# Performance work log

Hardware: AMD Instinct MI355X
Metric: run time of the kernel (lower is better)

## Reference

```python
import jax, jax.numpy as jnp
import numpy as np

D, NQ, BS, NL, NH, NP, DFF = 256, 900, 8, 4, 8, 4, 1024
HD = D // NH
SHAPES = np.array([[100, 100], [50, 50], [25, 25], [13, 13]], dtype=np.int64)  # (H, W) per level
LSTART = np.concatenate([[0], np.cumsum(SHAPES[:, 0] * SHAPES[:, 1])[:-1]]).astype(np.int64)
LMEM = int((SHAPES[:, 0] * SHAPES[:, 1]).sum())


def layer_norm(x, g, b, eps=1e-5):
    mu = x.mean(-1, keepdims=True)
    var = ((x - mu) ** 2).mean(-1, keepdims=True)
    return (x - mu) * jax.lax.rsqrt(var + eps) * g + b


def _forward(tgt, tgt_query_pos, tgt_reference_points, memory,
             in_proj_w, in_proj_b, out_proj_w, out_proj_b,
             samp_off_w, samp_off_b, attn_w_w, attn_w_b,
             value_proj_w, value_proj_b, output_proj_w, output_proj_b,
             lin1_w, lin1_b, lin2_w, lin2_b,
             norm1_g, norm1_b, norm2_g, norm2_b, norm3_g, norm3_b):
    # ---- self-attention (seq-first, torch nn.MultiheadAttention semantics) ----
    q = tgt + tgt_query_pos  # q = k = with_pos_embed(tgt, pos)
    Wq, Wk, Wv = jnp.split(in_proj_w, 3, 0)
    bq, bk, bv = jnp.split(in_proj_b, 3, 0)
    def heads(x):  # (nq, bs, d) -> (bs, nh, nq, hd)
        return x.reshape(NQ, BS, NH, HD).transpose(1, 2, 0, 3)
    qh = heads(q @ Wq.T + bq)
    kh = heads(q @ Wk.T + bk)
    vh = heads(tgt @ Wv.T + bv)
    attn = jax.nn.softmax(jnp.einsum('bhqd,bhkd->bhqk', qh, kh) / np.float32(np.sqrt(HD)), -1)
    sa = jnp.einsum('bhqk,bhkd->bhqd', attn, vh).transpose(2, 0, 1, 3).reshape(NQ, BS, D)
    sa = sa @ out_proj_w.T + out_proj_b
    t = layer_norm(tgt + sa, norm2_g, norm2_b)

    # ---- MSDeformAttn cross-attention (batch-first internally) ----
    qb = (t + tgt_query_pos).transpose(1, 0, 2)          # (bs, nq, d)
    refb = tgt_reference_points.transpose(1, 0, 2, 3)    # (bs, nq, nl, 2) in [0,1]
    memb = memory.transpose(1, 0, 2)                     # (bs, L, d)
    value = (memb @ value_proj_w.T + value_proj_b).reshape(BS, LMEM, NH, HD)
    off = (qb @ samp_off_w.T + samp_off_b).reshape(BS, NQ, NH, NL, NP, 2)
    aw = jax.nn.softmax((qb @ attn_w_w.T + attn_w_b).reshape(BS, NQ, NH, NL * NP), -1)
    aw = aw.reshape(BS, NQ, NH, NL, NP)
    normz = jnp.asarray(SHAPES[:, ::-1].copy(), dtype=jnp.float32)  # (nl, 2) = [W, H]
    loc = refb[:, :, None, :, None, :] + off / normz[None, None, None, :, None, :]

    out = jnp.zeros((BS, NQ, NH, HD), jnp.float32)
    for l in range(NL):  # fixed small number of pyramid levels
        Hl, Wl = int(SHAPES[l, 0]), int(SHAPES[l, 1])
        s = int(LSTART[l])
        v_l = value[:, s:s + Hl * Wl]  # (bs, Hl*Wl, nh, hd)
        # grid_sample(align_corners=False, padding=zeros) pixel coords
        x = (loc[:, :, :, l, :, 0] * Wl - 0.5).transpose(0, 1, 3, 2).reshape(BS, NQ * NP, NH)
        y = (loc[:, :, :, l, :, 1] * Hl - 0.5).transpose(0, 1, 3, 2).reshape(BS, NQ * NP, NH)
        x0 = jnp.floor(x)
        y0 = jnp.floor(y)
        samp = jnp.zeros((BS, NQ * NP, NH, HD), jnp.float32)
        for dx in (0, 1):
            for dy in (0, 1):
                xc = x0 + dx
                yc = y0 + dy
                w = (1.0 - jnp.abs(x - xc)) * (1.0 - jnp.abs(y - yc))
                valid = (xc >= 0) & (xc < Wl) & (yc >= 0) & (yc < Hl)
                idx = (jnp.clip(yc, 0, Hl - 1) * Wl + jnp.clip(xc, 0, Wl - 1)).astype(jnp.int32)
                g = jnp.take_along_axis(v_l, idx[..., None], axis=1)  # (bs, nq*np, nh, hd)
                samp = samp + jnp.where(valid, w, 0.0)[..., None] * g
        samp = samp.reshape(BS, NQ, NP, NH, HD)
        out = out + jnp.einsum('bqhp,bqphd->bqhd', aw[:, :, :, l], samp)
    ca = (out.reshape(BS, NQ, D) @ output_proj_w.T + output_proj_b).transpose(1, 0, 2)
    t = layer_norm(t + ca, norm1_g, norm1_b)

    # ---- FFN ----
    ffn = jax.nn.relu(t @ lin1_w.T + lin1_b) @ lin2_w.T + lin2_b
    return layer_norm(t + ffn, norm3_g, norm3_b)


def setup_inputs() -> dict:
    key = jax.random.key(0)
    ks = jax.random.split(key, 24)
    r = lambda i, shape, s: jax.random.normal(ks[i], shape, jnp.float32) * s
    return {
        'tgt': r(0, (NQ, BS, D), 1.0),
        'tgt_query_pos': r(1, (NQ, BS, D), 1.0),
        'tgt_reference_points': jax.random.uniform(ks[2], (NQ, BS, NL, 2), jnp.float32),
        'memory': r(3, (LMEM, BS, D), 1.0),
        'spatial_shapes': jnp.asarray(SHAPES),
        'level_start_index': jnp.asarray(LSTART),
        'in_proj_w': r(4, (3 * D, D), 0.02), 'in_proj_b': r(5, (3 * D,), 0.02),
        'out_proj_w': r(6, (D, D), 0.02), 'out_proj_b': r(7, (D,), 0.02),
        'samp_off_w': r(8, (NH * NL * NP * 2, D), 0.01), 'samp_off_b': r(9, (NH * NL * NP * 2,), 0.01),
        'attn_w_w': r(10, (NH * NL * NP, D), 0.02), 'attn_w_b': r(11, (NH * NL * NP,), 0.02),
        'value_proj_w': r(12, (D, D), 0.02), 'value_proj_b': r(13, (D,), 0.02),
        'output_proj_w': r(14, (D, D), 0.02), 'output_proj_b': r(15, (D,), 0.02),
        'lin1_w': r(16, (DFF, D), 0.02), 'lin1_b': r(17, (DFF,), 0.02),
        'lin2_w': r(18, (D, DFF), 0.02), 'lin2_b': r(19, (D,), 0.02),
        'norm1_g': jnp.ones((D,), jnp.float32), 'norm1_b': jnp.zeros((D,), jnp.float32),
        'norm2_g': jnp.ones((D,), jnp.float32), 'norm2_b': jnp.zeros((D,), jnp.float32),
        'norm3_g': jnp.ones((D,), jnp.float32), 'norm3_b': jnp.zeros((D,), jnp.float32),
    }


def reference(tgt, tgt_query_pos, tgt_reference_points, memory, spatial_shapes, level_start_index,
              in_proj_w, in_proj_b, out_proj_w, out_proj_b, samp_off_w, samp_off_b,
              attn_w_w, attn_w_b, value_proj_w, value_proj_b, output_proj_w, output_proj_b,
              lin1_w, lin1_b, lin2_w, lin2_b, norm1_g, norm1_b, norm2_g, norm2_b, norm3_g, norm3_b):
    # spatial_shapes / level_start_index are static level constants (module-level SHAPES/LSTART)
    return _forward(tgt, tgt_query_pos, tgt_reference_points, memory,
                    in_proj_w, in_proj_b, out_proj_w, out_proj_b,
                    samp_off_w, samp_off_b, attn_w_w, attn_w_b,
                    value_proj_w, value_proj_b, output_proj_w, output_proj_b,
                    lin1_w, lin1_b, lin2_w, lin2_b,
                    norm1_g, norm1_b, norm2_g, norm2_b, norm3_g, norm3_b)
```

## Files before the change

kernel.cpp:

```cpp
#include <hip/hip_runtime.h>
#include <hip/hip_bf16.h>


namespace {
constexpr int D_ = 256;
constexpr int NQ_ = 900;
constexpr int BS_ = 8;
constexpr int NH_ = 8;
constexpr int HD_ = 32;
constexpr int DFF_ = 1024;
constexpr int MTOK = NQ_ * BS_;
constexpr int LMEM_ = 13294;
constexpr long T = (long)MTOK * D_;
constexpr float QSC = 0.17677669529663687f;
constexpr int QKS = 512;
}

typedef __attribute__((ext_vector_type(8))) short bf8_t;
typedef __attribute__((ext_vector_type(4))) float f4_t;

#define MFMA16(a, b, c) __builtin_amdgcn_mfma_f32_16x16x32_bf16((a), (b), (c), 0, 0, 0)

__device__ __forceinline__ unsigned short bfbits(float x) {
    union { __hip_bfloat16 h; unsigned short u; } cv;
    cv.h = __float2bfloat16(x);
    return cv.u;
}
__device__ __forceinline__ float bf2f(unsigned short u) {
    union { float f; unsigned v; } cv;
    cv.v = ((unsigned)u) << 16;
    return cv.f;
}

__device__ __forceinline__ void gload16(const unsigned short* g, unsigned short* l) {
    __builtin_amdgcn_global_load_lds(
        (const __attribute__((address_space(1))) unsigned int*)(g),
        (__attribute__((address_space(3))) unsigned int*)(l), 16, 0, 0);
}

__global__ void prep_inputs(const float* __restrict__ tgt, const float* __restrict__ pos,
                            unsigned short* __restrict__ tgt_bf,
                            unsigned short* __restrict__ qplus_bf, long n4) {
    const long i = (long)blockIdx.x * blockDim.x + threadIdx.x;
    if (i < n4) {
        const float4 tv = ((const float4*)tgt)[i];
        const float4 pv = ((const float4*)pos)[i];
        union { unsigned short u[4]; uint2 w; } a, b;
        a.u[0] = bfbits(tv.x); a.u[1] = bfbits(tv.y); a.u[2] = bfbits(tv.z); a.u[3] = bfbits(tv.w);
        b.u[0] = bfbits(tv.x + pv.x); b.u[1] = bfbits(tv.y + pv.y);
        b.u[2] = bfbits(tv.z + pv.z); b.u[3] = bfbits(tv.w + pv.w);
        ((uint2*)tgt_bf)[i] = a.w;
        ((uint2*)qplus_bf)[i] = b.w;
    }
}

__global__ void permute_mem(const float* __restrict__ mem, unsigned short* __restrict__ dst) {
    const long idx = (long)blockIdx.x * 256 + threadIdx.x;
    const int d4 = (int)(idx & 63);
    const int b = (int)((idx >> 6) & 7);
    const long i = idx >> 9;
    const float4 v = ((const float4*)mem)[idx];
    union { unsigned short u[4]; uint2 w; } pk;
    pk.u[0] = bfbits(v.x); pk.u[1] = bfbits(v.y); pk.u[2] = bfbits(v.z); pk.u[3] = bfbits(v.w);
    *(uint2*)(dst + (((long)b * LMEM_ + i) * D_ + d4 * 4)) = pk.w;
}

__global__ void conv_weights(
    const float* __restrict__ ipw, const float* __restrict__ opw,
    const float* __restrict__ sow, const float* __restrict__ aww,
    const float* __restrict__ vpw, const float* __restrict__ outpw,
    const float* __restrict__ l1w, const float* __restrict__ l2w,
    const float* __restrict__ ipb, const float* __restrict__ sob,
    const float* __restrict__ awb,
    unsigned short* __restrict__ Wbf, float* __restrict__ biasAll)
{
    if (blockIdx.x == 0) {
        for (int j = threadIdx.x; j < 512; j += 256)
            biasAll[j] = (j < 256) ? ipb[j] * QSC : ipb[j];
        for (int j = threadIdx.x; j < 384; j += 256)
            biasAll[512 + j] = (j < 256) ? sob[j] : awb[j - 256];
    }
    const long idx4 = (long)blockIdx.x * 256 + threadIdx.x;
    if (idx4 >= 253952) return;
    const long e = idx4 * 4;
    const float* src; long off; float sc = 1.f;
    if (e < 196608)      { src = ipw;   off = 0;      if (e < 65536) sc = QSC; }
    else if (e < 262144) { src = opw;   off = 196608; }
    else if (e < 327680) { src = sow;   off = 262144; }
    else if (e < 360448) { src = aww;   off = 327680; }
    else if (e < 425984) { src = vpw;   off = 360448; }
    else if (e < 491520) { src = outpw; off = 425984; }
    else if (e < 753664) { src = l1w;   off = 491520; }
    else                 { src = l2w;   off = 753664; }
    const float4 v = *(const float4*)(src + (e - off));
    union { unsigned short u[4]; uint2 w; } pk;
    pk.u[0] = bfbits(v.x * sc); pk.u[1] = bfbits(v.y * sc);
    pk.u[2] = bfbits(v.z * sc); pk.u[3] = bfbits(v.w * sc);
    *(uint2*)(Wbf + e) = pk.w;
}

template<bool RELU, bool OUTBF16>
__global__ __launch_bounds__(256) void gemm_mfma(
    const unsigned short* __restrict__ A, const unsigned short* __restrict__ W,
    const float* __restrict__ bias, void* __restrict__ C, int M, int N, int K)
{
    __shared__ unsigned short As[128 * 32];
    __shared__ unsigned short Ws[128 * 32];
    const int t = threadIdx.x;
    const long m0 = (long)blockIdx.x * 128;
    const int n0 = blockIdx.y * 128;
    const int row0 = t >> 2, cg = t & 3;
    long ar0 = m0 + row0;        if (ar0 > M - 1) ar0 = M - 1;
    long ar1 = m0 + 64 + row0;   if (ar1 > M - 1) ar1 = M - 1;
    const unsigned short* ga0 = A + ar0 * K + cg * 8;
    const unsigned short* ga1 = A + ar1 * K + cg * 8;
    const unsigned short* gw0 = W + (long)(n0 + row0) * K + cg * 8;
    const unsigned short* gw1 = W + (long)(n0 + 64 + row0) * K + cg * 8;
    unsigned short* la0 = As + t * 8;
    unsigned short* la1 = As + 2048 + t * 8;
    unsigned short* lw0 = Ws + t * 8;
    unsigned short* lw1 = Ws + 2048 + t * 8;
    const int lane = t & 63, wave = t >> 6;
    const int c = lane & 15, g = lane >> 4;
    const int wr = wave >> 1, wc = wave & 1;
    f4_t acc[4][4];
#pragma unroll
    for (int i = 0; i < 4; ++i)
#pragma unroll
        for (int j = 0; j < 4; ++j)
            acc[i][j] = f4_t{0.f, 0.f, 0.f, 0.f};

    for (int kb = 0; kb < K; kb += 32) {
        gload16(ga0 + kb, la0);
        gload16(ga1 + kb, la1);
        gload16(gw0 + kb, lw0);
        gload16(gw1 + kb, lw1);
        __syncthreads();
        bf8_t af[4], bfr[4];
#pragma unroll
        for (int i = 0; i < 4; ++i) {
            af[i] = *(const bf8_t*)(As + (wr * 64 + i * 16 + c) * 32 + g * 8);
            bfr[i] = *(const bf8_t*)(Ws + (wc * 64 + i * 16 + c) * 32 + g * 8);
        }
#pragma unroll
        for (int i = 0; i < 4; ++i)
#pragma unroll
            for (int j = 0; j < 4; ++j)
                acc[i][j] = MFMA16(af[i], bfr[j], acc[i][j]);
        __syncthreads();
    }

#pragma unroll
    for (int i = 0; i < 4; ++i) {
        const long rbase = m0 + wr * 64 + i * 16 + 4 * g;
#pragma unroll
        for (int j = 0; j < 4; ++j) {
            const int col = n0 + wc * 64 + j * 16 + c;
            const float bv = bias[col];
#pragma unroll
            for (int r = 0; r < 4; ++r) {
                const long rr = rbase + r;
                if (rr < M) {
                    float v = acc[i][j][r] + bv;
                    if (RELU) v = fmaxf(v, 0.f);
                    if (OUTBF16) ((unsigned short*)C)[rr * N + col] = bfbits(v);
                    else         ((float*)C)[rr * N + col] = v;
                }
            }
        }
    }
}

__global__ __launch_bounds__(256) void attn_mfma(
    const unsigned short* __restrict__ Qb, const unsigned short* __restrict__ Kb,
    const unsigned short* __restrict__ Vb, unsigned short* __restrict__ sa)
{
    __shared__ float smemf[2112];
    unsigned short* Ks = (unsigned short*)smemf;
    unsigned short* Vt = (unsigned short*)(smemf + 1024);
    const int t = threadIdx.x;
    const int wave = t >> 6, lane = t & 63;
    const int g = lane >> 4, c = lane & 15;
    const int b = blockIdx.x >> 3, h = blockIdx.x & 7;
    const int q0 = blockIdx.y * 64 + wave * 16;
    const int q = q0 + c;
    const bool qv = q < NQ_;
    const bf8_t qf = *(const bf8_t*)(Qb + ((long)(qv ? q : 0) * BS_ + b) * QKS + h * HD_ + 8 * g);

    f4_t acc0 = {0.f, 0.f, 0.f, 0.f}, acc1 = {0.f, 0.f, 0.f, 0.f};
    float m_run = -1e30f, l_run = 0.f;
    const int sk = t >> 2, sd = (t & 3) * 8;

    for (int kc = 0; kc < NQ_; kc += 64) {
        __syncthreads();
        {
            const int key = kc + sk;
            union { bf8_t v; unsigned short u[8]; } kv, vv;
            if (key < NQ_) {
                kv.v = *(const bf8_t*)(Kb + ((long)key * BS_ + b) * QKS + h * HD_ + sd);
                vv.v = *(const bf8_t*)(Vb + ((long)key * BS_ + b) * D_ + h * HD_ + sd);
            } else {
#pragma unroll
                for (int u = 0; u < 8; ++u) { kv.u[u] = 0; vv.u[u] = 0; }
            }
            *(bf8_t*)(Ks + sk * 32 + sd) = kv.v;
#pragma unroll
            for (int u = 0; u < 8; ++u) {
                const int r = sd + u;
                Vt[r * 64 + (sk ^ ((r & 7) << 3))] = vv.u[u];
            }
        }
        __syncthreads();

        f4_t s[4];
#pragma unroll
        for (int tt = 0; tt < 4; ++tt) {
            const bf8_t kf = *(const bf8_t*)(Ks + (tt * 16 + c) * 32 + 8 * g);
            f4_t z = {0.f, 0.f, 0.f, 0.f};
            s[tt] = MFMA16(kf, qf, z);
        }
        float sv[16];
#pragma unroll
        for (int tt = 0; tt < 4; ++tt)
#pragma unroll
            for (int r = 0; r < 4; ++r) {
                float x = s[tt][r];
                if (kc + tt * 16 + 4 * g + r >= NQ_) x = -1e30f;
                sv[tt * 4 + r] = x;
            }
        float mloc = sv[0];
#pragma unroll
        for (int i = 1; i < 16; ++i) mloc = fmaxf(mloc, sv[i]);
        mloc = fmaxf(mloc, __shfl_xor(mloc, 16));
        mloc = fmaxf(mloc, __shfl_xor(mloc, 32));
        const float mnew = fmaxf(m_run, mloc);
        const float resc = __expf(m_run - mnew);
        float p[16], ls = 0.f;
#pragma unroll
        for (int i = 0; i < 16; ++i) { p[i] = __expf(sv[i] - mnew); ls += p[i]; }
        ls += __shfl_xor(ls, 16);
        ls += __shfl_xor(ls, 32);
        l_run = l_run * resc + ls;
        m_run = mnew;
#pragma unroll
        for (int r = 0; r < 4; ++r) { acc0[r] *= resc; acc1[r] *= resc; }

        unsigned pk[4][2];
#pragma unroll
        for (int tt = 0; tt < 4; ++tt) {
            pk[tt][0] = (unsigned)bfbits(p[tt * 4 + 0]) | ((unsigned)bfbits(p[tt * 4 + 1]) << 16);
            pk[tt][1] = (unsigned)bfbits(p[tt * 4 + 2]) | ((unsigned)bfbits(p[tt * 4 + 3]) << 16);
        }
        const int srcA = ((g & 1) << 5) + c;
        const int srcB = srcA + 16;
#pragma unroll
        for (int kh = 0; kh < 2; ++kh) {
            const unsigned a0 = __shfl(pk[kh * 2][0], srcA), b0_ = __shfl(pk[kh * 2 + 1][0], srcA);
            const unsigned a1 = __shfl(pk[kh * 2][1], srcA), b1_ = __shfl(pk[kh * 2 + 1][1], srcA);
            const unsigned a2 = __shfl(pk[kh * 2][0], srcB), b2_ = __shfl(pk[kh * 2 + 1][0], srcB);
            const unsigned a3 = __shfl(pk[kh * 2][1], srcB), b3_ = __shfl(pk[kh * 2 + 1][1], srcB);
            union { bf8_t v; unsigned u[4]; } pf;
            const bool hi = (g & 2);
            pf.u[0] = hi ? b0_ : a0; pf.u[1] = hi ? b1_ : a1;
            pf.u[2] = hi ? b2_ : a2; pf.u[3] = hi ? b3_ : a3;
            const int kcol = (kh * 32 + 8 * g) ^ ((c & 7) << 3);
            const bf8_t vf0 = *(const bf8_t*)(Vt + c * 64 + kcol);
            const bf8_t vf1 = *(const bf8_t*)(Vt + (16 + c) * 64 + kcol);
            acc0 = MFMA16(vf0, pf.v, acc0);
            acc1 = MFMA16(vf1, pf.v, acc1);
        }
    }

    __syncthreads();
    const float invl = 1.f / l_run;
    float* O = smemf + wave * 528;
#pragma unroll
    for (int r = 0; r < 4; ++r) {
        O[c * 33 + 4 * g + r] = acc0[r] * invl;
        O[c * 33 + 16 + 4 * g + r] = acc1[r] * invl;
    }
    __syncthreads();
    {
        const int ql = lane >> 2, part = lane & 3;
        const int qg = q0 + ql;
        if (qg < NQ_) {
            union { bf8_t v; unsigned short u[8]; } pk;
#pragma unroll
            for (int u = 0; u < 8; ++u) pk.u[u] = bfbits(O[ql * 33 + part * 8 + u]);
            *(bf8_t*)(sa + ((long)qg * BS_ + b) * D_ + h * HD_ + part * 8) = pk.v;
        }
    }
}

__global__ __launch_bounds__(256) void msdeform_kernel(
    const float* __restrict__ oa, const float* __restrict__ refp,
    const unsigned short* __restrict__ val, unsigned short* __restrict__ out)
{
    __shared__ float saw[128];
    __shared__ float redm[8], redi[8];
    __shared__ float swt[128][4];
    __shared__ int sidx[128][4];
    const int bq = blockIdx.x;
    const int b = bq / NQ_, q = bq % NQ_;
    const int t = threadIdx.x;
    if (t < 128) saw[t] = oa[(long)bq * 384 + 256 + t];
    __syncthreads();
    if (t < 8) {
        float mx = -1e30f;
        for (int i = 0; i < 16; ++i) mx = fmaxf(mx, saw[t * 16 + i]);
        float s = 0.f;
        for (int i = 0; i < 16; ++i) s += __expf(saw[t * 16 + i] - mx);
        redm[t] = mx; redi[t] = 1.f / s;
    }
    __syncthreads();
    if (t < 128) {
        const int h = t >> 4, lp = t & 15, l = lp >> 2, p = lp & 3;
        const float aw = __expf(saw[t] - redm[h]) * redi[h];
        const int Wi = (l == 0) ? 100 : (l == 1) ? 50 : (l == 2) ? 25 : 13;
        const int Hi = Wi;
        const int sl = (l == 0) ? 0 : (l == 1) ? 10000 : (l == 2) ? 12500 : 13125;
        const float offx = oa[(long)bq * 384 + h * 32 + l * 8 + p * 2 + 0];
        const float offy = oa[(long)bq * 384 + h * 32 + l * 8 + p * 2 + 1];
        const float refx = refp[(((long)q * BS_ + b) * 4 + l) * 2 + 0];
        const float refy = refp[(((long)q * BS_ + b) * 4 + l) * 2 + 1];
        const float fW = (float)Wi, fH = (float)Hi;
        const float x = (refx + offx / fW) * fW - 0.5f;
        const float y = (refy + offy / fH) * fH - 0.5f;
        const float x0f = floorf(x), y0f = floorf(y);
        const float fx = x - x0f, fy = y - y0f;
        const int ix = (int)x0f, iy = (int)y0f;
        const float wts[4] = {(1.f - fx) * (1.f - fy), fx * (1.f - fy),
                              (1.f - fx) * fy,          fx * fy};
        const int xs[4] = {ix, ix + 1, ix, ix + 1};
        const int ys[4] = {iy, iy, iy + 1, iy + 1};
#pragma unroll
        for (int tap = 0; tap < 4; ++tap) {
            const bool valid = (xs[tap] >= 0) & (xs[tap] < Wi) & (ys[tap] >= 0) & (ys[tap] < Hi);
            const int xc = min(max(xs[tap], 0), Wi - 1);
            const int yc = min(max(ys[tap], 0), Hi - 1);
            swt[t][tap] = valid ? aw * wts[tap] : 0.f;
            sidx[t][tap] = b * LMEM_ + sl + yc * Wi + xc;
        }
    }
    __syncthreads();
    const int h = t >> 5, r = t & 31, qd = r & 7, s = r >> 3;
    float a0 = 0.f, a1 = 0.f, a2 = 0.f, a3 = 0.f;
#pragma unroll
    for (int i = 0; i < 16; ++i) {
        const int j = h * 16 + i;
        const float wv = swt[j][s];
        const long base = (long)sidx[j][s] * D_ + h * HD_ + qd * 4;
        const uint2 raw = *(const uint2*)(val + base);
        a0 += wv * bf2f((unsigned short)(raw.x & 0xffff));
        a1 += wv * bf2f((unsigned short)(raw.x >> 16));
        a2 += wv * bf2f((unsigned short)(raw.y & 0xffff));
        a3 += wv * bf2f((unsigned short)(raw.y >> 16));
    }
    a0 += __shfl_xor(a0, 8); a0 += __shfl_xor(a0, 16);
    a1 += __shfl_xor(a1, 8); a1 += __shfl_xor(a1, 16);
    a2 += __shfl_xor(a2, 8); a2 += __shfl_xor(a2, 16);
    a3 += __shfl_xor(a3, 8); a3 += __shfl_xor(a3, 16);
    if (s == 0) {
        union { unsigned short u[4]; uint2 w; } pk;
        pk.u[0] = bfbits(a0); pk.u[1] = bfbits(a1); pk.u[2] = bfbits(a2); pk.u[3] = bfbits(a3);
        *(uint2*)(out + (long)bq * D_ + h * HD_ + qd * 4) = pk.w;
    }
}

__global__ __launch_bounds__(256) void ln_kernel(
    const float* __restrict__ inA, const float* __restrict__ inB,
    const float* __restrict__ g, const float* __restrict__ be,
    float* __restrict__ out, const float* __restrict__ pos,
    unsigned short* __restrict__ bfOut, int swapB, int bfMode)
{
    const int r = blockIdx.x * 4 + (threadIdx.x >> 6);
    const int lane = threadIdx.x & 63;
    long rb = r;
    if (swapB) rb = (long)(r & 7) * NQ_ + (r >> 3);
    const float4 a4 = *(const float4*)(inA + (long)r * D_ + lane * 4);
    const float4 b4 = *(const float4*)(inB + rb * D_ + lane * 4);
    float x[4] = {a4.x + b4.x, a4.y + b4.y, a4.z + b4.z, a4.w + b4.w};
    float s = x[0] + x[1] + x[2] + x[3];
#pragma unroll
    for (int off = 32; off > 0; off >>= 1) s += __shfl_xor(s, off);
    const float mu = s * (1.f / D_);
    float v = 0.f;
#pragma unroll
    for (int cc = 0; cc < 4; ++cc) { const float dd = x[cc] - mu; v += dd * dd; }
#pragma unroll
    for (int off = 32; off > 0; off >>= 1) v += __shfl_xor(v, off);
    const float rs = rsqrtf(v * (1.f / D_) + 1e-5f);
    const float4 g4 = *(const float4*)(g + lane * 4);
    const float4 e4 = *(const float4*)(be + lane * 4);
    const float gg[4] = {g4.x, g4.y, g4.z, g4.w};
    const float ee[4] = {e4.x, e4.y, e4.z, e4.w};
    float y[4];
#pragma unroll
    for (int cc = 0; cc < 4; ++cc) y[cc] = (x[cc] - mu) * rs * gg[cc] + ee[cc];
    *(float4*)(out + (long)r * D_ + lane * 4) = make_float4(y[0], y[1], y[2], y[3]);
    if (bfMode) {
        float z[4] = {y[0], y[1], y[2], y[3]};
        long er = r;
        if (bfMode == 2) {
            const float4 p4 = *(const float4*)(pos + (long)r * D_ + lane * 4);
            z[0] += p4.x; z[1] += p4.y; z[2] += p4.z; z[3] += p4.w;
            er = (long)(r & 7) * NQ_ + (r >> 3);
        }
        union { unsigned short u[4]; uint2 w; } pk;
        pk.u[0] = bfbits(z[0]); pk.u[1] = bfbits(z[1]);
        pk.u[2] = bfbits(z[2]); pk.u[3] = bfbits(z[3]);
        *(uint2*)(bfOut + er * D_ + lane * 4) = pk.w;
    }
}

extern "C" void kernel_launch(void* const* d_in, const int* in_sizes, int n_in,
                              void* d_out, int out_size, void* d_ws, size_t ws_size,
                              hipStream_t stream) {
    const float* tgt   = (const float*)d_in[0];
    const float* pos   = (const float*)d_in[1];
    const float* refp  = (const float*)d_in[2];
    const float* mem   = (const float*)d_in[3];
    const float* ipw   = (const float*)d_in[6];
    const float* ipb   = (const float*)d_in[7];
    const float* opw   = (const float*)d_in[8];
    const float* opb   = (const float*)d_in[9];
    const float* sow   = (const float*)d_in[10];
    const float* sob   = (const float*)d_in[11];
    const float* aww   = (const float*)d_in[12];
    const float* awb   = (const float*)d_in[13];
    const float* vpw   = (const float*)d_in[14];
    const float* vpb   = (const float*)d_in[15];
    const float* outpw = (const float*)d_in[16];
    const float* outpb = (const float*)d_in[17];
    const float* l1w   = (const float*)d_in[18];
    const float* l1b   = (const float*)d_in[19];
    const float* l2w   = (const float*)d_in[20];
    const float* l2b   = (const float*)d_in[21];
    const float* n1g = (const float*)d_in[22]; const float* n1be = (const float*)d_in[23];
    const float* n2g = (const float*)d_in[24]; const float* n2be = (const float*)d_in[25];
    const float* n3g = (const float*)d_in[26]; const float* n3be = (const float*)d_in[27];

    char* wsb = (char*)d_ws;
    auto alloc = [&](size_t bytes) { char* p = wsb; wsb += (bytes + 255) & ~(size_t)255; return p; };
    unsigned short* Wbf      = (unsigned short*)alloc(1015808 * 2);
    float*          biasAll  = (float*)alloc(896 * 4);
    unsigned short* tgt_bf   = (unsigned short*)alloc(T * 2);
    unsigned short* qplus_bf = (unsigned short*)alloc(T * 2);
    unsigned short* QK_bf    = (unsigned short*)alloc(T * 4);
    unsigned short* Vb_bf    = (unsigned short*)alloc(T * 2);
    unsigned short* sa_bf    = (unsigned short*)alloc(T * 2);
    float*          saproj   = (float*)alloc(T * 4);
    float*          t1       = (float*)alloc(T * 4);
    unsigned short* memT     = (unsigned short*)alloc((long)BS_ * LMEM_ * D_ * 2);
    unsigned short* val      = (unsigned short*)alloc((long)BS_ * LMEM_ * D_ * 2);
    unsigned short* qplus2_bf = qplus_bf;
    unsigned short* sampo_bf  = tgt_bf;
    float*          oa        = (float*)sa_bf;
    float*          t2        = (float*)(QK_bf + T);
    unsigned short* t2_bf     = QK_bf;
    unsigned short* ffnh_bf   = memT;
    float*          ffno      = (float*)((char*)memT + (long)MTOK * DFF_ * 2);
    float*          ca        = (float*)((char*)ffno + T * 4);
    const unsigned short* wqk = Wbf + 0;
    const unsigned short* wv  = Wbf + 131072;
    const unsigned short* wo  = Wbf + 196608;
    const unsigned short* wsoaw = Wbf + 262144;
    const unsigned short* wvp = Wbf + 360448;
    const unsigned short* wop = Wbf + 425984;
    const unsigned short* wl1 = Wbf + 491520;
    const unsigned short* wl2 = Wbf + 753664;
    const float* bias_qk = biasAll;
    const float* bias_oa = biasAll + 512;

    const dim3 blk(256);
    const dim3 g_m(57, 2);

    conv_weights<<<992, blk, 0, stream>>>(ipw, opw, sow, aww, vpw, outpw, l1w, l2w,
                                          ipb, sob, awb, Wbf, biasAll);
    prep_inputs<<<1800, blk, 0, stream>>>(tgt, pos, tgt_bf, qplus_bf, T / 4);
    permute_mem<<<26588, blk, 0, stream>>>(mem, memT);
    gemm_mfma<false, true><<<dim3(57, 4), blk, 0, stream>>>(qplus_bf, wqk, bias_qk, QK_bf, MTOK, QKS, D_);
    gemm_mfma<false, true><<<g_m, blk, 0, stream>>>(tgt_bf, wv, ipb + 2 * D_, Vb_bf, MTOK, D_, D_);
    attn_mfma<<<dim3(64, 15), blk, 0, stream>>>(QK_bf, QK_bf + 256, Vb_bf, sa_bf);
    gemm_mfma<false, false><<<g_m, blk, 0, stream>>>(sa_bf, wo, opb, saproj, MTOK, D_, D_);
    ln_kernel<<<1800, blk, 0, stream>>>(tgt, saproj, n2g, n2be, t1, pos, qplus2_bf, 0, 2);
    gemm_mfma<false, true><<<dim3(831, 2), blk, 0, stream>>>(memT, wvp, vpb, val, BS_ * LMEM_, D_, D_);
    gemm_mfma<false, false><<<dim3(57, 3), blk, 0, stream>>>(qplus2_bf, wsoaw, bias_oa, oa, MTOK, 384, D_);
    msdeform_kernel<<<7200, blk, 0, stream>>>(oa, refp, val, sampo_bf);
    gemm_mfma<false, false><<<g_m, blk, 0, stream>>>(sampo_bf, wop, outpb, ca, MTOK, D_, D_);
    ln_kernel<<<1800, blk, 0, stream>>>(t1, ca, n1g, n1be, t2, nullptr, t2_bf, 1, 1);
    gemm_mfma<true, true><<<dim3(57, 8), blk, 0, stream>>>(t2_bf, wl1, l1b, ffnh_bf, MTOK, DFF_, D_);
    gemm_mfma<false, false><<<g_m, blk, 0, stream>>>(ffnh_bf, wl2, l2b, ffno, MTOK, D_, DFF_);
    ln_kernel<<<1800, blk, 0, stream>>>(t2, ffno, n3g, n3be, (float*)d_out, nullptr, nullptr, 0, 0);
}
```

Measured before the change: 272.9 us.

## Fuse fp32-to-bf16 input conversion and memory permute into GEMM A-loading

Adds a GEMM variant that reads fp32 activations directly, optionally adds a second input (tgt+pos), converts to bf16 in registers and stores to LDS. Its strided row mapping absorbs the seq-first to batch-first memory permute. This removes the prep_inputs and permute_mem kernels and their bf16 intermediate round trips. The cost is that A tiles now go through registers without async LDS loads and read twice the bytes (fp32), which may stall the GEMM main loop. The workspace is also reorganised into non-aliased buffers.

```diff
diff --git a/kernel.cpp b/kernel.cpp
--- a/kernel.cpp
+++ b/kernel.cpp
@@ -36,33 +36,6 @@
     __builtin_amdgcn_global_load_lds(
         (const __attribute__((address_space(1))) unsigned int*)(g),
         (__attribute__((address_space(3))) unsigned int*)(l), 16, 0, 0);
-}
-
-__global__ void prep_inputs(const float* __restrict__ tgt, const float* __restrict__ pos,
-                            unsigned short* __restrict__ tgt_bf,
-                            unsigned short* __restrict__ qplus_bf, long n4) {
-    const long i = (long)blockIdx.x * blockDim.x + threadIdx.x;
-    if (i < n4) {
-        const float4 tv = ((const float4*)tgt)[i];
-        const float4 pv = ((const float4*)pos)[i];
-        union { unsigned short u[4]; uint2 w; } a, b;
-        a.u[0] = bfbits(tv.x); a.u[1] = bfbits(tv.y); a.u[2] = bfbits(tv.z); a.u[3] = bfbits(tv.w);
-        b.u[0] = bfbits(tv.x + pv.x); b.u[1] = bfbits(tv.y + pv.y);
-        b.u[2] = bfbits(tv.z + pv.z); b.u[3] = bfbits(tv.w + pv.w);
-        ((uint2*)tgt_bf)[i] = a.w;
-        ((uint2*)qplus_bf)[i] = b.w;
-    }
-}
-
-__global__ void permute_mem(const float* __restrict__ mem, unsigned short* __restrict__ dst) {
-    const long idx = (long)blockIdx.x * 256 + threadIdx.x;
-    const int d4 = (int)(idx & 63);
-    const int b = (int)((idx >> 6) & 7);
-    const long i = idx >> 9;
-    const float4 v = ((const float4*)mem)[idx];
-    union { unsigned short u[4]; uint2 w; } pk;
-    pk.u[0] = bfbits(v.x); pk.u[1] = bfbits(v.y); pk.u[2] = bfbits(v.z); pk.u[3] = bfbits(v.w);
-    *(uint2*)(dst + (((long)b * LMEM_ + i) * D_ + d4 * 4)) = pk.w;
 }
 
 __global__ void conv_weights(
@@ -163,6 +136,101 @@
                 if (rr < M) {
                     float v = acc[i][j][r] + bv;
                     if (RELU) v = fmaxf(v, 0.f);
+                    if (OUTBF16) ((unsigned short*)C)[rr * N + col] = bfbits(v);
+                    else         ((float*)C)[rr * N + col] = v;
+                }
+            }
+        }
+    }
+}
+
+template<bool OUTBF16>
+__global__ __launch_bounds__(256) void gemm_f32a(
+    const float* __restrict__ A, const float* __restrict__ A2,
+    const unsigned short* __restrict__ W, const float* __restrict__ bias,
+    void* __restrict__ C, int M, int N, int K, int R1, int S1, int S2)
+{
+    __shared__ unsigned short As[128 * 32];
+    __shared__ unsigned short Ws[128 * 32];
+    const int t = threadIdx.x;
+    const long m0 = (long)blockIdx.x * 128;
+    const int n0 = blockIdx.y * 128;
+    const int row0 = t >> 2, cg = t & 3;
+    int gr0 = (int)m0 + row0;       if (gr0 > M - 1) gr0 = M - 1;
+    int gr1 = (int)m0 + 64 + row0;  if (gr1 > M - 1) gr1 = M - 1;
+    const long ar0 = (long)(gr0 / R1) * S1 + (long)(gr0 % R1) * S2;
+    const long ar1 = (long)(gr1 / R1) * S1 + (long)(gr1 % R1) * S2;
+    const float* Ap0 = A + ar0 * K + cg * 8;
+    const float* Ap1 = A + ar1 * K + cg * 8;
+    const float* Bp0 = A2 ? A2 + ar0 * K + cg * 8 : nullptr;
+    const float* Bp1 = A2 ? A2 + ar1 * K + cg * 8 : nullptr;
+    const unsigned short* gw0 = W + (long)(n0 + row0) * K + cg * 8;
+    const unsigned short* gw1 = W + (long)(n0 + 64 + row0) * K + cg * 8;
+    unsigned short* la0 = As + row0 * 32 + cg * 8;
+    unsigned short* la1 = As + (64 + row0) * 32 + cg * 8;
+    unsigned short* lw0 = Ws + t * 8;
+    unsigned short* lw1 = Ws + 2048 + t * 8;
+    const int lane = t & 63, wave = t >> 6;
+    const int c = lane & 15, g = lane >> 4;
+    const int wr = wave >> 1, wc = wave & 1;
+    f4_t acc[4][4];
+#pragma unroll
+    for (int i = 0; i < 4; ++i)
+#pragma unroll
+        for (int j = 0; j < 4; ++j)
+            acc[i][j] = f4_t{0.f, 0.f, 0.f, 0.f};
+
+    for (int kb = 0; kb < K; kb += 32) {
+        gload16(gw0 + kb, lw0);
+        gload16(gw1 + kb, lw1);
+        float4 a00 = *(const float4*)(Ap0 + kb);
+        float4 a01 = *(const float4*)(Ap0 + kb + 4);
+        float4 a10 = *(const float4*)(Ap1 + kb);
+        float4 a11 = *(const float4*)(Ap1 + kb + 4);
+        if (A2) {
+            const float4 b00 = *(const float4*)(Bp0 + kb);
+            const float4 b01 = *(const float4*)(Bp0 + kb + 4);
+            const float4 b10 = *(const float4*)(Bp1 + kb);
+            const float4 b11 = *(const float4*)(Bp1 + kb + 4);
+            a00.x += b00.x; a00.y += b00.y; a00.z += b00.z; a00.w += b00.w;
+            a01.x += b01.x; a01.y += b01.y; a01.z += b01.z; a01.w += b01.w;
+            a10.x += b10.x; a10.y += b10.y; a10.z += b10.z; a10.w += b10.w;
+            a11.x += b11.x; a11.y += b11.y; a11.z += b11.z; a11.w += b11.w;
+        }
+        union { bf8_t v; unsigned short u[8]; } p0, p1;
+        p0.u[0] = bfbits(a00.x); p0.u[1] = bfbits(a00.y); p0.u[2] = bfbits(a00.z); p0.u[3] = bfbits(a00.w);
+        p0.u[4] = bfbits(a01.x); p0.u[5] = bfbits(a01.y); p0.u[6] = bfbits(a01.z); p0.u[7] = bfbits(a01.w);
+        p1.u[0] = bfbits(a10.x); p1.u[1] = bfbits(a10.y); p1.u[2] = bfbits(a10.z); p1.u[3] = bfbits(a10.w);
+        p1.u[4] = bfbits(a11.x); p1.u[5] = bfbits(a11.y); p1.u[6] = bfbits(a11.z); p1.u[7] = bfbits(a11.w);
+        *(bf8_t*)la0 = p0.v;
+        *(bf8_t*)la1 = p1.v;
+        __syncthreads();
+        bf8_t af[4], bfr[4];
+#pragma unroll
+        for (int i = 0; i < 4; ++i) {
+            af[i] = *(const bf8_t*)(As + (wr * 64 + i * 16 + c) * 32 + g * 8);
+            bfr[i] = *(const bf8_t*)(Ws + (wc * 64 + i * 16 + c) * 32 + g * 8);
+        }
+#pragma unroll
+        for (int i = 0; i < 4; ++i)
+#pragma unroll
+            for (int j = 0; j < 4; ++j)
+                acc[i][j] = MFMA16(af[i], bfr[j], acc[i][j]);
+        __syncthreads();
+    }
+
+#pragma unroll
+    for (int i = 0; i < 4; ++i) {
+        const long rbase = m0 + wr * 64 + i * 16 + 4 * g;
+#pragma unroll
+        for (int j = 0; j < 4; ++j) {
+            const int col = n0 + wc * 64 + j * 16 + c;
+            const float bv = bias[col];
+#pragma unroll
+            for (int r = 0; r < 4; ++r) {
+                const long rr = rbase + r;
+                if (rr < M) {
+                    float v = acc[i][j][r] + bv;
                     if (OUTBF16) ((unsigned short*)C)[rr * N + col] = bfbits(v);
                     else         ((float*)C)[rr * N + col] = v;
                 }
@@ -442,33 +510,30 @@
 
     char* wsb = (char*)d_ws;
     auto alloc = [&](size_t bytes) { char* p = wsb; wsb += (bytes + 255) & ~(size_t)255; return p; };
-    unsigned short* Wbf      = (unsigned short*)alloc(1015808 * 2);
-    float*          biasAll  = (float*)alloc(896 * 4);
-    unsigned short* tgt_bf   = (unsigned short*)alloc(T * 2);
-    unsigned short* qplus_bf = (unsigned short*)alloc(T * 2);
-    unsigned short* QK_bf    = (unsigned short*)alloc(T * 4);
-    unsigned short* Vb_bf    = (unsigned short*)alloc(T * 2);
-    unsigned short* sa_bf    = (unsigned short*)alloc(T * 2);
-    float*          saproj   = (float*)alloc(T * 4);
-    float*          t1       = (float*)alloc(T * 4);
-    unsigned short* memT     = (unsigned short*)alloc((long)BS_ * LMEM_ * D_ * 2);
-    unsigned short* val      = (unsigned short*)alloc((long)BS_ * LMEM_ * D_ * 2);
-    unsigned short* qplus2_bf = qplus_bf;
-    unsigned short* sampo_bf  = tgt_bf;
-    float*          oa        = (float*)sa_bf;
-    float*          t2        = (float*)(QK_bf + T);
-    unsigned short* t2_bf     = QK_bf;
-    unsigned short* ffnh_bf   = memT;
-    float*          ffno      = (float*)((char*)memT + (long)MTOK * DFF_ * 2);
-    float*          ca        = (float*)((char*)ffno + T * 4);
-    const unsigned short* wqk = Wbf + 0;
-    const unsigned short* wv  = Wbf + 131072;
-    const unsigned short* wo  = Wbf + 196608;
+    unsigned short* Wbf       = (unsigned short*)alloc(1015808 * 2);
+    float*          biasAll   = (float*)alloc(896 * 4);
+    unsigned short* QK_bf     = (unsigned short*)alloc(T * 4);
+    unsigned short* Vb_bf     = (unsigned short*)alloc(T * 2);
+    unsigned short* sa_bf     = (unsigned short*)alloc(T * 2);
+    float*          saproj    = (float*)alloc(T * 4);
+    float*          t1        = (float*)alloc(T * 4);
+    unsigned short* qplus2_bf = (unsigned short*)alloc(T * 2);
+    float*          oa        = (float*)alloc((long)MTOK * 384 * 4);
+    unsigned short* sampo_bf  = (unsigned short*)alloc(T * 2);
+    float*          ca        = (float*)alloc(T * 4);
+    float*          t2        = (float*)alloc(T * 4);
+    unsigned short* t2_bf     = (unsigned short*)alloc(T * 2);
+    unsigned short* ffnh_bf   = (unsigned short*)alloc((long)MTOK * DFF_ * 2);
+    float*          ffno      = (float*)alloc(T * 4);
+    unsigned short* val       = (unsigned short*)alloc((long)BS_ * LMEM_ * D_ * 2);
+    const unsigned short* wqk   = Wbf + 0;
+    const unsigned short* wv    = Wbf + 131072;
+    const unsigned short* wo    = Wbf + 196608;
     const unsigned short* wsoaw = Wbf + 262144;
-    const unsigned short* wvp = Wbf + 360448;
-    const unsigned short* wop = Wbf + 425984;
-    const unsigned short* wl1 = Wbf + 491520;
-    const unsigned short* wl2 = Wbf + 753664;
+    const unsigned short* wvp   = Wbf + 360448;
+    const unsigned short* wop   = Wbf + 425984;
+    const unsigned short* wl1   = Wbf + 491520;
+    const unsigned short* wl2   = Wbf + 753664;
     const float* bias_qk = biasAll;
     const float* bias_oa = biasAll + 512;
 
@@ -477,14 +542,15 @@
 
     conv_weights<<<992, blk, 0, stream>>>(ipw, opw, sow, aww, vpw, outpw, l1w, l2w,
                                           ipb, sob, awb, Wbf, biasAll);
-    prep_inputs<<<1800, blk, 0, stream>>>(tgt, pos, tgt_bf, qplus_bf, T / 4);
-    permute_mem<<<26588, blk, 0, stream>>>(mem, memT);
-    gemm_mfma<false, true><<<dim3(57, 4), blk, 0, stream>>>(qplus_bf, wqk, bias_qk, QK_bf, MTOK, QKS, D_);
-    gemm_mfma<false, true><<<g_m, blk, 0, stream>>>(tgt_bf, wv, ipb + 2 * D_, Vb_bf, MTOK, D_, D_);
+    gemm_f32a<true><<<dim3(57, 4), blk, 0, stream>>>(tgt, pos, wqk, bias_qk, QK_bf,
+                                                     MTOK, QKS, D_, MTOK, 0, 1);
+    gemm_f32a<true><<<g_m, blk, 0, stream>>>(tgt, nullptr, wv, ipb + 2 * D_, Vb_bf,
+                                             MTOK, D_, D_, MTOK, 0, 1);
     attn_mfma<<<dim3(64, 15), blk, 0, stream>>>(QK_bf, QK_bf + 256, Vb_bf, sa_bf);
     gemm_mfma<false, false><<<g_m, blk, 0, stream>>>(sa_bf, wo, opb, saproj, MTOK, D_, D_);
     ln_kernel<<<1800, blk, 0, stream>>>(tgt, saproj, n2g, n2be, t1, pos, qplus2_bf, 0, 2);
-    gemm_mfma<false, true><<<dim3(831, 2), blk, 0, stream>>>(memT, wvp, vpb, val, BS_ * LMEM_, D_, D_);
+    gemm_f32a<true><<<dim3(831, 2), blk, 0, stream>>>(mem, nullptr, wvp, vpb, val,
+                                                      BS_ * LMEM_, D_, D_, LMEM_, 1, BS_);
     gemm_mfma<false, false><<<dim3(57, 3), blk, 0, stream>>>(qplus2_bf, wsoaw, bias_oa, oa, MTOK, 384, D_);
     msdeform_kernel<<<7200, blk, 0, stream>>>(oa, refp, val, sampo_bf);
     gemm_mfma<false, false><<<g_m, blk, 0, stream>>>(sampo_bf, wop, outpb, ca, MTOK, D_, D_);
```

Measured after the change: 258.5 us. -5.3%, faster.
